# Kernel optimization log

Hardware: AMD Instinct MI355X
Metric: run time of the kernel (lower is better)

The kernel has to match this reference:

```python
import jax, jax.numpy as jnp
import numpy as np

NB = 5          # LC kernel size (odd -> L_out == L with pad = NB//2)
S = 8           # num_sparse_LC segments
N_LEVELS = 4
K_DENSE = 3
K_LC = 3
SQ = np.float32(np.sqrt(0.5))


def haar_dec(x):
    # level-1 haar wavedec, periodization mode; x: (..., L), L even
    x0, x1 = x[..., 0::2], x[..., 1::2]
    return (x0 + x1) * SQ, (x0 - x1) * SQ  # (cA, cD)


def haar_rec(cA, cD):
    # inverse of haar_dec
    x0 = (cA + cD) * SQ
    x1 = (cA - cD) * SQ
    return jnp.stack([x0, x1], axis=-1).reshape(cA.shape[:-1] + (-1,))


def lc_apply(x, w, b):
    # cheapPartiallyUnsharedConv1d. x: (B,d,k,2,L); w: (d,k,o=2,i=2,S,NB); b: (d,k,2,S)
    L = x.shape[-1]
    p = NB // 2
    xp = jnp.pad(x, ((0, 0),) * 4 + ((p, p),))
    idx = jnp.arange(L)[:, None] + jnp.arange(NB)[None, :]      # (L, NB)
    patches = xp[..., idx]                                      # (B,d,k,2,L,NB)
    # per-segment weights: floor(L/S) repeats per segment, remainder -> last segment
    R = L // S
    seg = jnp.clip(jnp.arange(L) // R, 0, S - 1)                # (L,)
    wf = w[:, :, :, :, seg, :]                                  # (d,k,o,i,L,NB)
    bf = b[:, :, :, seg]                                        # (d,k,o,L)
    return jnp.einsum('dkoilf,bdkilf->bdkol', wf, patches) + bf


def lin_deriv(ts, ys, t):
    # derivative of linear interpolation of ys over knots ts, evaluated at t
    # ts: (T,); ys: (B,T,D); t: (T,) -> (B,T,D)
    i = jnp.clip(jnp.searchsorted(ts, t, side='right') - 1, 0, ts.shape[0] - 2)
    return (ys[:, i + 1, :] - ys[:, i, :]) / (ts[i + 1] - ts[i])[None, :, None]


def setup_inputs() -> dict:
    key = jax.random.key(0)
    ks = jax.random.split(key, 8)
    B, L, D, d, k = 16, 2048, 64, 32, 16
    dn = L >> N_LEVELS  # 128 == dense_dim
    seq = jax.random.normal(ks[0], (B, L, D), jnp.float32)
    coeffs = jax.random.normal(ks[1], (B, L, D), jnp.float32)
    time_step = jnp.arange(L, dtype=jnp.float32)
    time = jnp.arange(L, dtype=jnp.float32)
    Wg = jax.random.normal(ks[2], (D, d), jnp.float32) * (2.0 / D) ** 0.5
    Wh = jax.random.normal(ks[3], (d, D * k), jnp.float32) * (2.0 / d) ** 0.5
    dense_W = jax.random.normal(ks[4], (K_DENSE, d, k, dn, dn), jnp.float32) * (2.0 / dn) ** 0.5
    lc_w = jax.random.normal(ks[5], (N_LEVELS, K_LC, d, k, 2, 2, S, NB), jnp.float32) * (2.0 / (2 * NB)) ** 0.5
    lc_b = jax.random.uniform(ks[6], (N_LEVELS, K_LC, d, k, 2, S), jnp.float32)
    Wrev = jax.random.normal(ks[7], (d, D), jnp.float32) * (2.0 / d) ** 0.5
    return dict(seq=seq, coeffs=coeffs, time=time, time_step=time_step,
                Wg=Wg, Wh=Wh, dense_W=dense_W, lc_w=lc_w, lc_b=lc_b, Wrev=Wrev)


def reference(seq, coeffs, time, time_step, Wg, Wh, dense_W, lc_w, lc_b, Wrev):
    B, L, D = seq.shape
    d = Wg.shape[1]
    k = Wh.shape[1] // D
    der = lin_deriv(time_step, coeffs, time)                    # (B,L,D) == der_X.squeeze(-1)
    z = jax.nn.relu(seq @ Wg)                                   # (B,L,d)
    h = jax.nn.relu(z @ Wh).reshape(B, L, D, k)                 # (B,L,D,k)
    v = jnp.einsum('blDk,blD->bkl', h, der)                     # (B,k,L)

    # analysis: n_levels of level-1 haar wavedec
    ca = v
    details, approxs = [], []
    for _ in range(N_LEVELS):
        ca, cd = haar_dec(ca)
        details.append(cd)
        approxs.append(ca)

    # coarsest approx -> per-(d,k) dense stack
    cur = jnp.tile(approxs[-1][:, None, :, :], (1, d, 1, 1))    # (B,d,k,dn)
    for j in range(K_DENSE):
        cur = jnp.einsum('dktq,bdkq->bdkt', dense_W[j], cur)

    # synthesis with locally-connected refinements
    for l in reversed(range(N_LEVELS)):
        chi = jnp.tile(jnp.stack([details[l], approxs[l]], axis=2)[:, None],
                       (1, d, 1, 1, 1))                          # (B,d,k,2,Ll)
        for j in range(K_LC):
            chi = jax.nn.relu(lc_apply(chi, lc_w[l, j], lc_b[l, j]))
        # shape_correction is identity: lengths match exactly with haar/pow2
        X = chi.at[:, :, :, 1, :].add(cur)                       # add approx on channel 1
        cur = haar_rec(X[:, :, :, 1, :], X[:, :, :, 0, :])       # (B,d,k,2*Ll)

    out = jnp.sum(cur, axis=2)                                   # (B,d,L)
    U = jnp.transpose(out, (0, 2, 1)) @ Wrev                     # (B,L,D_out)
    return U
```

## Files before the change

kernel.cpp:

```cpp
#include <hip/hip_runtime.h>

#define SQC 0.70710678118654752f

typedef __attribute__((ext_vector_type(8))) short bf16x8;
typedef __attribute__((ext_vector_type(4))) float f32x4;

__device__ __forceinline__ unsigned short bf16_rne(float x) {
  unsigned int u = __float_as_uint(x);
  u += 0x7FFFu + ((u >> 16) & 1u);
  return (unsigned short)(u >> 16);
}

__global__ __launch_bounds__(256) void k_prep(const float* __restrict__ Wh,
                                              unsigned short* __restrict__ WhT) {
  int i = blockIdx.x * 256 + threadIdx.x;
  int n = i >> 5, dd = i & 31;
  WhT[i] = bf16_rne(Wh[dd * 1024 + n]);
}

__global__ __launch_bounds__(256) void k_prep_w(const float* __restrict__ lcw,
                                                const float* __restrict__ lcb,
                                                float* __restrict__ re) {
  int g = blockIdx.x * 256 + threadIdx.x;
  int l = g / 294912;
  int r1 = g - l * 294912;
  int dk = r1 / 576;
  int i = r1 - dk * 576;
  int j = i / 192;
  int r = i - j * 192;
  int sg = r / 24;
  int t = r - sg * 24;
  float val = 0.f;
  if (t < 20) {
    int oi = t / 5, f = t - oi * 5;
    val = lcw[((size_t)(l * 3 + j) * 512 + dk) * 160 + (oi * 8 + sg) * 5 + f];
  } else if (t < 22) {
    val = lcb[((size_t)(l * 3 + j) * 512 + dk) * 16 + (t - 20) * 8 + sg];
  }
  re[g] = val;
}

__global__ __launch_bounds__(256) void k_z(const float* __restrict__ seq,
                                           const float* __restrict__ Wg,
                                           unsigned short* __restrict__ zout) {
  int t = (blockIdx.x >> 2) * 256 + threadIdx.x;
  int dq = blockIdx.x & 3;
  const float4* srow = (const float4*)(seq + (size_t)t * 64);
  float acc[8];
#pragma unroll
  for (int i = 0; i < 8; ++i) acc[i] = 0.f;
#pragma unroll 4
  for (int D4 = 0; D4 < 16; ++D4) {
    float4 s4 = srow[D4];
    const float* sp = (const float*)&s4;
#pragma unroll
    for (int q = 0; q < 4; ++q) {
      float s = sp[q];
      int D = D4 * 4 + q;
      const float* wr = Wg + D * 32 + dq * 8;
#pragma unroll
      for (int d = 0; d < 8; ++d) acc[d] = fmaf(s, wr[d], acc[d]);
    }
  }
  uint4 o;
  unsigned int* op = (unsigned int*)&o;
#pragma unroll
  for (int i = 0; i < 4; ++i) {
    unsigned int lo = bf16_rne(fmaxf(acc[2 * i], 0.f));
    unsigned int hi = bf16_rne(fmaxf(acc[2 * i + 1], 0.f));
    op[i] = lo | (hi << 16);
  }
  *(uint4*)(zout + (size_t)t * 32 + dq * 8) = o;
}

__global__ __launch_bounds__(256) void k_v(const unsigned short* __restrict__ zb_g,
                                           const float* __restrict__ coeffs,
                                           const unsigned short* __restrict__ WhT,
                                           float* __restrict__ v) {
  __shared__ unsigned short zs[64][40];
  __shared__ float ders[64][68];
  __shared__ float vout[16][68];
  const int tid = threadIdx.x;
  const int b = blockIdx.x >> 5;
  const int lblk = (blockIdx.x & 31) * 64;
  const unsigned int* zrow_g =
      (const unsigned int*)(zb_g + ((size_t)b * 2048 + lblk) * 32);
  for (int i = tid; i < 1024; i += 256) {
    int r = i >> 4, c2 = i & 15;
    *(unsigned int*)&zs[r][c2 * 2] = zrow_g[i];
  }
  for (int i = tid; i < 4096; i += 256) {
    int r = i >> 6, D = i & 63;
    int ii = min(lblk + r, 2046);
    const float* c0 = coeffs + ((size_t)b * 2048 + ii) * 64 + D;
    ders[r][D] = c0[64] - c0[0];
  }
  __syncthreads();
  const int lane = tid & 63;
  const int wv = tid >> 6;
  const int col = lane & 15, quad = lane >> 4;
  bf16x8 afrag = *(bf16x8*)&zs[wv * 16 + col][quad * 8];
  f32x4 vacc = {0.f, 0.f, 0.f, 0.f};
  const unsigned short* bptr = WhT + col * 32 + quad * 8;
  const int lrow0 = wv * 16 + quad * 4;
#pragma unroll 4
  for (int t = 0; t < 64; ++t) {
    bf16x8 bfrag = *(const bf16x8*)(bptr + t * 512);
    f32x4 c = {0.f, 0.f, 0.f, 0.f};
    c = __builtin_amdgcn_mfma_f32_16x16x32_bf16(afrag, bfrag, c, 0, 0, 0);
#pragma unroll
    for (int r = 0; r < 4; ++r)
      vacc[r] = fmaf(fmaxf(c[r], 0.f), ders[lrow0 + r][t], vacc[r]);
  }
#pragma unroll
  for (int r = 0; r < 4; ++r) vout[col][lrow0 + r] = vacc[r];
  __syncthreads();
  for (int i = tid; i < 1024; i += 256) {
    int kk = i >> 6, ll = i & 63;
    v[((size_t)b * 16 + kk) * 2048 + lblk + ll] = vout[kk][ll];
  }
}

__global__ __launch_bounds__(256) void k_haar(const float* __restrict__ v,
                                              float* __restrict__ wdet,
                                              float* __restrict__ wapp,
                                              float* __restrict__ a0T) {
  __shared__ float buf[2048];
  __shared__ float buf2[1024];
  int bk = blockIdx.x;
  const float* src = v + (size_t)bk * 2048;
  for (int i = threadIdx.x; i < 2048; i += 256) buf[i] = src[i];
  __syncthreads();
  int len = 1024;
  for (int l = 0; l < 4; ++l) {
    size_t off = (size_t)bk * 1920 + (2048 - (2048 >> l));
    for (int p = threadIdx.x; p < len; p += 256) {
      float a = buf[2 * p], c = buf[2 * p + 1];
      float cA = (a + c) * SQC, cD = (a - c) * SQC;
      buf2[p] = cA;
      wdet[off + p] = cD;
      wapp[off + p] = cA;
    }
    __syncthreads();
    for (int p = threadIdx.x; p < len; p += 256) buf[p] = buf2[p];
    __syncthreads();
    len >>= 1;
  }
  if (threadIdx.x < 128) {
    int k = bk & 15, bb = bk >> 4;
    a0T[((size_t)k * 128 + threadIdx.x) * 16 + bb] = buf[threadIdx.x];
  }
}

__global__ __launch_bounds__(256) void k_dense3(const float* __restrict__ dW,
                                                const float* __restrict__ a0T,
                                                float* __restrict__ curd) {
  __shared__ float bufA[128 * 20];
  __shared__ float bufB[128 * 20];
  const int tid = threadIdx.x;
  const int dk = blockIdx.x;
  const int d = dk >> 4, k = dk & 15;
  {
    const float* src = a0T + (size_t)k * 2048;
    for (int i = tid; i < 2048; i += 256) {
      int q = i >> 4, b = i & 15;
      bufA[q * 20 + b] = src[i];
    }
  }
  const int t = tid & 127;
  const int bh = (tid >> 7) << 3;
  float acc[8];
  float* bin = bufA;
  float* bout = bufB;
#pragma unroll 1
  for (int j = 0; j < 3; ++j) {
    __syncthreads();
    const float* Wt = dW + ((size_t)j * 512 + dk) * 16384 + (size_t)t * 128;
#pragma unroll
    for (int i = 0; i < 8; ++i) acc[i] = 0.f;
#pragma unroll 4
    for (int q4 = 0; q4 < 32; ++q4) {
      float4 wv4 = ((const float4*)Wt)[q4];
      const float* wp = (const float*)&wv4;
#pragma unroll
      for (int qq = 0; qq < 4; ++qq) {
        int q = q4 * 4 + qq;
        float w = wp[qq];
        const float* ar = bin + q * 20 + bh;
        float4 a0 = *(const float4*)(ar);
        float4 a1 = *(const float4*)(ar + 4);
        acc[0] = fmaf(w, a0.x, acc[0]); acc[1] = fmaf(w, a0.y, acc[1]);
        acc[2] = fmaf(w, a0.z, acc[2]); acc[3] = fmaf(w, a0.w, acc[3]);
        acc[4] = fmaf(w, a1.x, acc[4]); acc[5] = fmaf(w, a1.y, acc[5]);
        acc[6] = fmaf(w, a1.z, acc[6]); acc[7] = fmaf(w, a1.w, acc[7]);
      }
    }
    if (j < 2) {
      float* orow = bout + t * 20 + bh;
      *(float4*)orow = make_float4(acc[0], acc[1], acc[2], acc[3]);
      *(float4*)(orow + 4) = make_float4(acc[4], acc[5], acc[6], acc[7]);
      float* tmp = bin; bin = bout; bout = tmp;
    }
  }
#pragma unroll
  for (int i = 0; i < 8; ++i) {
    int b = bh + i;
    curd[(((size_t)b * 32 + d) * 16 + k) * 128 + t] = acc[i];
  }
}

__device__ __forceinline__ void loadw24(float (&wl)[24], const float* p) {
#pragma unroll
  for (int i = 0; i < 6; ++i) *(float4*)&wl[4 * i] = *(const float4*)(p + 4 * i);
}

template <int P>
__device__ __forceinline__ void conv_inplace(int lane, const float (&wl)[24],
                                             float (&x0)[P], float (&x1)[P]) {
  float l00 = __shfl_up(x0[P - 2], 1), l01 = __shfl_up(x0[P - 1], 1);
  float l10 = __shfl_up(x1[P - 2], 1), l11 = __shfl_up(x1[P - 1], 1);
  float r00 = __shfl_down(x0[0], 1), r01 = __shfl_down(x0[1], 1);
  float r10 = __shfl_down(x1[0], 1), r11 = __shfl_down(x1[1], 1);
  if (lane == 0) { l00 = 0.f; l01 = 0.f; l10 = 0.f; l11 = 0.f; }
  if (lane == 63) { r00 = 0.f; r01 = 0.f; r10 = 0.f; r11 = 0.f; }
  float a0 = l00, b0 = l01, a1 = l10, b1 = l11;
#pragma unroll
  for (int i = 0; i < P; ++i) {
    float c0 = x0[i], c1 = x1[i];
    float d0 = (i + 1 < P) ? x0[i + 1] : r00;
    float d1 = (i + 1 < P) ? x1[i + 1] : r10;
    float e0 = (i + 2 < P) ? x0[i + 2] : ((i + 2 == P) ? r00 : r01);
    float e1 = (i + 2 < P) ? x1[i + 2] : ((i + 2 == P) ? r10 : r11);
    float o0 = wl[20], o1 = wl[21];
    o0 = fmaf(wl[0], a0, o0); o0 = fmaf(wl[1], b0, o0); o0 = fmaf(wl[2], c0, o0);
    o0 = fmaf(wl[3], d0, o0); o0 = fmaf(wl[4], e0, o0);
    o0 = fmaf(wl[5], a1, o0); o0 = fmaf(wl[6], b1, o0); o0 = fmaf(wl[7], c1, o0);
    o0 = fmaf(wl[8], d1, o0); o0 = fmaf(wl[9], e1, o0);
    o1 = fmaf(wl[10], a0, o1); o1 = fmaf(wl[11], b0, o1); o1 = fmaf(wl[12], c0, o1);
    o1 = fmaf(wl[13], d0, o1); o1 = fmaf(wl[14], e0, o1);
    o1 = fmaf(wl[15], a1, o1); o1 = fmaf(wl[16], b1, o1); o1 = fmaf(wl[17], c1, o1);
    o1 = fmaf(wl[18], d1, o1); o1 = fmaf(wl[19], e1, o1);
    a0 = b0; b0 = c0; a1 = b1; b1 = c1;
    x0[i] = fmaxf(o0, 0.f);
    x1[i] = fmaxf(o1, 0.f);
  }
}

template <int P>
__device__ __forceinline__ void conv3(int lane, const float* wb, int seg,
                                      float (&x0)[P], float (&x1)[P]) {
  float wl[24];
  loadw24(wl, wb + (0 * 8 + seg) * 24);
  conv_inplace<P>(lane, wl, x0, x1);
  loadw24(wl, wb + (1 * 8 + seg) * 24);
  conv_inplace<P>(lane, wl, x0, x1);
  loadw24(wl, wb + (2 * 8 + seg) * 24);
  conv_inplace<P>(lane, wl, x0, x1);
}

template <int P>
__device__ __forceinline__ void haar_rec_reg(const float (&x0)[P], const float (&x1)[P],
                                             const float (&cur)[P], float (&nxt)[2 * P]) {
#pragma unroll
  for (int i = 0; i < P; ++i) {
    float X1 = x1[i] + cur[i], X0 = x0[i];
    nxt[2 * i] = (X1 + X0) * SQC;
    nxt[2 * i + 1] = (X1 - X0) * SQC;
  }
}

template <int P>
__device__ __forceinline__ void load_chi(const float* __restrict__ wdet,
                                         const float* __restrict__ wapp,
                                         size_t off, float (&x0)[P], float (&x1)[P]) {
#pragma unroll
  for (int i = 0; i < P; i += 2) {
    *(float2*)&x0[i] = *(const float2*)(wdet + off + i);
    *(float2*)&x1[i] = *(const float2*)(wapp + off + i);
  }
}

__global__ __launch_bounds__(256, 2) void k_lc(const float* __restrict__ wdet,
                                               const float* __restrict__ wapp,
                                               const float* __restrict__ curd,
                                               const float* __restrict__ lcw_re,
                                               float* __restrict__ osum01,
                                               float* __restrict__ osum23) {
  __shared__ float wbuf[4][584];
  __shared__ float accb[2][2112];
  const int tid = threadIdx.x;
  const int lane = tid & 63;
  const int wv = tid >> 6;
  const int kg = blockIdx.x & 3;
  const int d = (blockIdx.x >> 2) & 31;
  const int b = blockIdx.x >> 7;
  const int k = kg * 4 + wv;
  const int bk = b * 16 + k;
  const int dk = d * 16 + k;
  const int seg = lane >> 3;
  float* wb = wbuf[wv];

  auto stage_w = [&](int l) {
    const float4* src = (const float4*)(lcw_re + ((size_t)(l * 512) + dk) * 576);
    float4* dst = (float4*)wb;
#pragma unroll
    for (int ii = 0; ii < 3; ++ii) {
      int idx = lane + 64 * ii;
      if (idx < 144) dst[idx] = src[idx];
    }
  };

  float cur4[4];
  {
    float x0[2], x1[2], c3[2];
    stage_w(3);
    load_chi<2>(wdet, wapp, (size_t)bk * 1920 + 1792 + lane * 2, x0, x1);
    *(float2*)&c3[0] = *(const float2*)(curd + (((size_t)b * 32 + d) * 16 + k) * 128 + lane * 2);
    conv3<2>(lane, wb, seg, x0, x1);
    haar_rec_reg<2>(x0, x1, c3, cur4);
  }
  float cur8[8];
  {
    float x0[4], x1[4];
    stage_w(2);
    load_chi<4>(wdet, wapp, (size_t)bk * 1920 + 1536 + lane * 4, x0, x1);
    conv3<4>(lane, wb, seg, x0, x1);
    haar_rec_reg<4>(x0, x1, cur4, cur8);
  }
  float cur16[16];
  {
    float x0[8], x1[8];
    stage_w(1);
    load_chi<8>(wdet, wapp, (size_t)bk * 1920 + 1024 + lane * 8, x0, x1);
    conv3<8>(lane, wb, seg, x0, x1);
    haar_rec_reg<8>(x0, x1, cur8, cur16);
  }
  {
    float x0[16], x1[16];
    stage_w(0);
    load_chi<16>(wdet, wapp, (size_t)bk * 1920 + lane * 16, x0, x1);
    conv3<16>(lane, wb, seg, x0, x1);
    float* arow = &accb[wv & 1][lane * 33];
    if (wv >= 2) {
#pragma unroll
      for (int i = 0; i < 16; ++i) {
        float X1 = x1[i] + cur16[i], X0 = x0[i];
        arow[2 * i] = (X1 + X0) * SQC;
        arow[2 * i + 1] = (X1 - X0) * SQC;
      }
    }
    __syncthreads();
    if (wv < 2) {
#pragma unroll
      for (int i = 0; i < 16; ++i) {
        float X1 = x1[i] + cur16[i], X0 = x0[i];
        arow[2 * i] += (X1 + X0) * SQC;
        arow[2 * i + 1] += (X1 - X0) * SQC;
      }
    }
  }
  __syncthreads();
  float* obase = (kg < 2) ? osum01 : osum23;
  float* orow = obase + ((size_t)(kg & 1) * 512 + (size_t)b * 32 + d) * 2048;
#pragma unroll
  for (int r = 0; r < 8; ++r) {
    int p = r * 256 + tid;
    int L = p >> 5, J = p & 31;
    int a = L * 33 + J;
    orow[p] = accb[0][a] + accb[1][a];
  }
}

__global__ __launch_bounds__(256) void k_final(const float* __restrict__ osum01,
                                               const float* __restrict__ osum23,
                                               const float* __restrict__ Wrev,
                                               float* __restrict__ U) {
  int t = (blockIdx.x >> 2) * 256 + threadIdx.x;
  int Dq = blockIdx.x & 3;
  int b = t >> 11, l = t & 2047;
  float acc[16];
#pragma unroll
  for (int i = 0; i < 16; ++i) acc[i] = 0.f;
  for (int dd = 0; dd < 32; ++dd) {
    size_t off = ((size_t)b * 32 + dd) * 2048 + l;
    float x = osum01[off] + osum01[off + 1048576] +
              osum23[off] + osum23[off + 1048576];
    const float* wr = Wrev + dd * 64 + Dq * 16;
#pragma unroll
    for (int j = 0; j < 16; ++j) acc[j] = fmaf(x, wr[j], acc[j]);
  }
  float* o = U + (size_t)t * 64 + Dq * 16;
#pragma unroll
  for (int i = 0; i < 4; ++i)
    *(float4*)(o + 4 * i) =
        make_float4(acc[4 * i], acc[4 * i + 1], acc[4 * i + 2], acc[4 * i + 3]);
}

extern "C" void kernel_launch(void* const* d_in, const int* in_sizes, int n_in,
                              void* d_out, int out_size, void* d_ws, size_t ws_size,
                              hipStream_t stream) {
  const float* seq    = (const float*)d_in[0];
  const float* coeffs = (const float*)d_in[1];
  const float* Wg   = (const float*)d_in[4];
  const float* Wh   = (const float*)d_in[5];
  const float* dW   = (const float*)d_in[6];
  const float* lcw  = (const float*)d_in[7];
  const float* lcb  = (const float*)d_in[8];
  const float* Wrev = (const float*)d_in[9];
  float* out = (float*)d_out;

  float* w      = (float*)d_ws;
  unsigned short* zb16 = (unsigned short*)(w + 0);
  float* v      = w + 1048576;
  float* a0T    = w + 1572864;
  unsigned short* WhT = (unsigned short*)(w + 1572864 + 16384);
  float* lcw_re = w + 1605632;
  float* curd   = w + 3702784;
  float* osum01 = w + 4751360;
  float* wdet   = w + 6848512;
  float* wapp   = w + 7340032;
  float* osum23 = w + 7831552;

  k_prep<<<128, 256, 0, stream>>>(Wh, WhT);
  k_prep_w<<<4608, 256, 0, stream>>>(lcw, lcb, lcw_re);
  k_z<<<512, 256, 0, stream>>>(seq, Wg, zb16);
  k_v<<<512, 256, 0, stream>>>(zb16, coeffs, WhT, v);
  k_haar<<<256, 256, 0, stream>>>(v, wdet, wapp, a0T);
  k_dense3<<<512, 256, 0, stream>>>(dW, a0T, curd);
  k_lc<<<2048, 256, 0, stream>>>(wdet, wapp, curd, lcw_re, osum01, osum23);
  k_final<<<512, 256, 0, stream>>>(osum01, osum23, Wrev, out);
}
```

Baseline: 258.5 us.

## Merge prep kernels, load LC weights directly from global, split FMA chains

The two weight-preparation kernels are merged into a single launch that branches on block index. The LC kernel no longer stages per-wave weights into shared memory and reads each lane's segment weights straight from global memory. Weight loads for the smaller levels are prefetched one layer ahead. Each conv output's single FMA chain is split into two independent partial sums to shorten dependency latency. This removes a launch and the shared-memory staging, at the cost of more global or L2 weight traffic and higher register pressure.

```diff
diff --git a/kernel.cpp b/kernel.cpp
--- a/kernel.cpp
+++ b/kernel.cpp
@@ -11,17 +11,19 @@
   return (unsigned short)(u >> 16);
 }
 
-__global__ __launch_bounds__(256) void k_prep(const float* __restrict__ Wh,
-                                              unsigned short* __restrict__ WhT) {
-  int i = blockIdx.x * 256 + threadIdx.x;
-  int n = i >> 5, dd = i & 31;
-  WhT[i] = bf16_rne(Wh[dd * 1024 + n]);
-}
-
-__global__ __launch_bounds__(256) void k_prep_w(const float* __restrict__ lcw,
-                                                const float* __restrict__ lcb,
-                                                float* __restrict__ re) {
-  int g = blockIdx.x * 256 + threadIdx.x;
+__global__ __launch_bounds__(256) void k_prep_all(const float* __restrict__ Wh,
+                                                  unsigned short* __restrict__ WhT,
+                                                  const float* __restrict__ lcw,
+                                                  const float* __restrict__ lcb,
+                                                  float* __restrict__ re) {
+  int bid = blockIdx.x;
+  if (bid < 128) {
+    int i = bid * 256 + threadIdx.x;
+    int n = i >> 5, dd = i & 31;
+    WhT[i] = bf16_rne(Wh[dd * 1024 + n]);
+    return;
+  }
+  int g = (bid - 128) * 256 + threadIdx.x;
   int l = g / 294912;
   int r1 = g - l * 294912;
   int dk = r1 / 576;
@@ -231,31 +233,44 @@
     float d1 = (i + 1 < P) ? x1[i + 1] : r10;
     float e0 = (i + 2 < P) ? x0[i + 2] : ((i + 2 == P) ? r00 : r01);
     float e1 = (i + 2 < P) ? x1[i + 2] : ((i + 2 == P) ? r10 : r11);
-    float o0 = wl[20], o1 = wl[21];
-    o0 = fmaf(wl[0], a0, o0); o0 = fmaf(wl[1], b0, o0); o0 = fmaf(wl[2], c0, o0);
-    o0 = fmaf(wl[3], d0, o0); o0 = fmaf(wl[4], e0, o0);
-    o0 = fmaf(wl[5], a1, o0); o0 = fmaf(wl[6], b1, o0); o0 = fmaf(wl[7], c1, o0);
-    o0 = fmaf(wl[8], d1, o0); o0 = fmaf(wl[9], e1, o0);
-    o1 = fmaf(wl[10], a0, o1); o1 = fmaf(wl[11], b0, o1); o1 = fmaf(wl[12], c0, o1);
-    o1 = fmaf(wl[13], d0, o1); o1 = fmaf(wl[14], e0, o1);
-    o1 = fmaf(wl[15], a1, o1); o1 = fmaf(wl[16], b1, o1); o1 = fmaf(wl[17], c1, o1);
-    o1 = fmaf(wl[18], d1, o1); o1 = fmaf(wl[19], e1, o1);
+    float oa = fmaf(wl[0], a0, wl[20]);
+    float ob = wl[5] * a1;
+    float pa = fmaf(wl[10], a0, wl[21]);
+    float pb = wl[15] * a1;
+    oa = fmaf(wl[1], b0, oa);  ob = fmaf(wl[6], b1, ob);
+    pa = fmaf(wl[11], b0, pa); pb = fmaf(wl[16], b1, pb);
+    oa = fmaf(wl[2], c0, oa);  ob = fmaf(wl[7], c1, ob);
+    pa = fmaf(wl[12], c0, pa); pb = fmaf(wl[17], c1, pb);
+    oa = fmaf(wl[3], d0, oa);  ob = fmaf(wl[8], d1, ob);
+    pa = fmaf(wl[13], d0, pa); pb = fmaf(wl[18], d1, pb);
+    oa = fmaf(wl[4], e0, oa);  ob = fmaf(wl[9], e1, ob);
+    pa = fmaf(wl[14], e0, pa); pb = fmaf(wl[19], e1, pb);
     a0 = b0; b0 = c0; a1 = b1; b1 = c1;
-    x0[i] = fmaxf(o0, 0.f);
-    x1[i] = fmaxf(o1, 0.f);
+    x0[i] = fmaxf(oa + ob, 0.f);
+    x1[i] = fmaxf(pa + pb, 0.f);
   }
 }
 
 template <int P>
-__device__ __forceinline__ void conv3(int lane, const float* wb, int seg,
-                                      float (&x0)[P], float (&x1)[P]) {
-  float wl[24];
-  loadw24(wl, wb + (0 * 8 + seg) * 24);
-  conv_inplace<P>(lane, wl, x0, x1);
-  loadw24(wl, wb + (1 * 8 + seg) * 24);
-  conv_inplace<P>(lane, wl, x0, x1);
-  loadw24(wl, wb + (2 * 8 + seg) * 24);
-  conv_inplace<P>(lane, wl, x0, x1);
+__device__ __forceinline__ void conv3g(int lane, const float* __restrict__ wL,
+                                       float (&x0)[P], float (&x1)[P]) {
+  if constexpr (P >= 16) {
+    float wA[24];
+    loadw24(wA, wL);
+    conv_inplace<P>(lane, wA, x0, x1);
+    loadw24(wA, wL + 192);
+    conv_inplace<P>(lane, wA, x0, x1);
+    loadw24(wA, wL + 384);
+    conv_inplace<P>(lane, wA, x0, x1);
+  } else {
+    float wA[24], wB[24];
+    loadw24(wA, wL);
+    loadw24(wB, wL + 192);
+    conv_inplace<P>(lane, wA, x0, x1);
+    loadw24(wA, wL + 384);
+    conv_inplace<P>(lane, wB, x0, x1);
+    conv_inplace<P>(lane, wA, x0, x1);
+  }
 }
 
 template <int P>
@@ -286,7 +301,6 @@
                                                const float* __restrict__ lcw_re,
                                                float* __restrict__ osum01,
                                                float* __restrict__ osum23) {
-  __shared__ float wbuf[4][584];
   __shared__ float accb[2][2112];
   const int tid = threadIdx.x;
   const int lane = tid & 63;
@@ -298,48 +312,34 @@
   const int bk = b * 16 + k;
   const int dk = d * 16 + k;
   const int seg = lane >> 3;
-  float* wb = wbuf[wv];
-
-  auto stage_w = [&](int l) {
-    const float4* src = (const float4*)(lcw_re + ((size_t)(l * 512) + dk) * 576);
-    float4* dst = (float4*)wb;
-#pragma unroll
-    for (int ii = 0; ii < 3; ++ii) {
-      int idx = lane + 64 * ii;
-      if (idx < 144) dst[idx] = src[idx];
-    }
-  };
+  const float* wseg = lcw_re + (size_t)dk * 576 + seg * 24;
 
   float cur4[4];
   {
     float x0[2], x1[2], c3[2];
-    stage_w(3);
     load_chi<2>(wdet, wapp, (size_t)bk * 1920 + 1792 + lane * 2, x0, x1);
     *(float2*)&c3[0] = *(const float2*)(curd + (((size_t)b * 32 + d) * 16 + k) * 128 + lane * 2);
-    conv3<2>(lane, wb, seg, x0, x1);
+    conv3g<2>(lane, wseg + 3 * 294912, x0, x1);
     haar_rec_reg<2>(x0, x1, c3, cur4);
   }
   float cur8[8];
   {
     float x0[4], x1[4];
-    stage_w(2);
     load_chi<4>(wdet, wapp, (size_t)bk * 1920 + 1536 + lane * 4, x0, x1);
-    conv3<4>(lane, wb, seg, x0, x1);
+    conv3g<4>(lane, wseg + 2 * 294912, x0, x1);
     haar_rec_reg<4>(x0, x1, cur4, cur8);
   }
   float cur16[16];
   {
     float x0[8], x1[8];
-    stage_w(1);
     load_chi<8>(wdet, wapp, (size_t)bk * 1920 + 1024 + lane * 8, x0, x1);
-    conv3<8>(lane, wb, seg, x0, x1);
+    conv3g<8>(lane, wseg + 1 * 294912, x0, x1);
     haar_rec_reg<8>(x0, x1, cur8, cur16);
   }
   {
     float x0[16], x1[16];
-    stage_w(0);
     load_chi<16>(wdet, wapp, (size_t)bk * 1920 + lane * 16, x0, x1);
-    conv3<16>(lane, wb, seg, x0, x1);
+    conv3g<16>(lane, wseg, x0, x1);
     float* arow = &accb[wv & 1][lane * 33];
     if (wv >= 2) {
 #pragma unroll
@@ -421,8 +421,7 @@
   float* wapp   = w + 7340032;
   float* osum23 = w + 7831552;
 
-  k_prep<<<128, 256, 0, stream>>>(Wh, WhT);
-  k_prep_w<<<4608, 256, 0, stream>>>(lcw, lcb, lcw_re);
+  k_prep_all<<<4736, 256, 0, stream>>>(Wh, WhT, lcw, lcb, lcw_re);
   k_z<<<512, 256, 0, stream>>>(seq, Wg, zb16);
   k_v<<<512, 256, 0, stream>>>(zb16, coeffs, WhT, v);
   k_haar<<<256, 256, 0, stream>>>(v, wdet, wapp, a0T);
```

Result: slower. 265.9 us (+2.9%).
